# Kernel tuning notes

Measured on AMD Instinct MI355X. Metric: run time of the kernel, lower is better.

## Reference

```python
import jax, jax.numpy as jnp
import numpy as np

EMBED_DIM = 1152
NUM_HEADS = 16
HEAD_DIM = EMBED_DIM // NUM_HEADS
SCALE = HEAD_DIM ** -0.5


def setup_inputs() -> dict:
    key = jax.random.key(0)
    ks = jax.random.split(key, 9)
    B, N, D = 8, 1024, EMBED_DIM
    s = (2.0 / D) ** 0.5
    return {
        "hidden_states": jax.random.normal(ks[0], (B, N, D), dtype=jnp.float32),
        "q_w": jax.random.normal(ks[1], (D, D), dtype=jnp.float32) * s,
        "q_b": jnp.zeros((D,), dtype=jnp.float32),
        "k_w": jax.random.normal(ks[2], (D, D), dtype=jnp.float32) * s,
        "k_b": jnp.zeros((D,), dtype=jnp.float32),
        "v_w": jax.random.normal(ks[3], (D, D), dtype=jnp.float32) * s,
        "v_b": jnp.zeros((D,), dtype=jnp.float32),
        "o_w": jax.random.normal(ks[4], (D, D), dtype=jnp.float32) * s,
        "o_b": jnp.zeros((D,), dtype=jnp.float32),
    }


def reference(hidden_states, q_w, q_b, k_w, k_b, v_w, v_b, o_w, o_b):
    B, N, D = hidden_states.shape
    H, Hd = NUM_HEADS, HEAD_DIM
    # Linear layers: torch nn.Linear stores weight [out, in]; y = x @ W^T + b
    q = hidden_states @ q_w.T + q_b
    k = hidden_states @ k_w.T + k_b
    v = hidden_states @ v_w.T + v_b
    # [B, N, H, Hd] -> [B, H, N, Hd]
    q = q.reshape(B, N, H, Hd).transpose(0, 2, 1, 3)
    k = k.reshape(B, N, H, Hd).transpose(0, 2, 1, 3)
    v = v.reshape(B, N, H, Hd).transpose(0, 2, 1, 3)
    scores = jnp.einsum("bhqd,bhkd->bhqk", q, k) * SCALE
    attn_probs = jax.nn.softmax(scores, axis=-1)
    # dropout p=0.0 (eval) -> identity
    out = jnp.einsum("bhqk,bhkd->bhqd", attn_probs, v)
    out = out.transpose(0, 2, 1, 3).reshape(B, N, D)
    out = out @ o_w.T + o_b
    return (out, attn_probs)
```

## Files before the change

### kernel.cpp

```cpp
#include <hip/hip_runtime.h>

typedef _Float16 half_t;
typedef __attribute__((ext_vector_type(8))) _Float16 half8;
typedef __attribute__((ext_vector_type(4))) _Float16 half4;
typedef __attribute__((ext_vector_type(4))) float f32x4;

#define MFMA16(a, b, c) __builtin_amdgcn_mfma_f32_16x16x32_f16((a), (b), (c), 0, 0, 0)

__global__ void cvt_f16(const float* __restrict__ src, half_t* __restrict__ dst) {
  int i = (blockIdx.x * 256 + threadIdx.x) * 4;
  float4 v = *(const float4*)(src + i);
  half4 o = { (half_t)v.x, (half_t)v.y, (half_t)v.z, (half_t)v.w };
  *(half4*)(dst + i) = o;
}

__global__ __launch_bounds__(256, 2) void gemm_qkv(
    const half_t* __restrict__ X,
    const half_t* __restrict__ Wq, const half_t* __restrict__ Wk, const half_t* __restrict__ Wv,
    const float* __restrict__ bq, const float* __restrict__ bk, const float* __restrict__ bv,
    half_t* __restrict__ qo, half_t* __restrict__ ko, half_t* __restrict__ vo)
{
  __shared__ half_t As[128 * 40];
  __shared__ half_t Bs[128 * 40];
  const int t = threadIdx.x;
  const int w = t >> 6, L = t & 63, quad = L >> 4, c16 = L & 15;
  const int m0 = blockIdx.x * 128;
  const int by = blockIdx.y;
  const int mat = by / 9;
  const int f0 = (by - mat * 9) * 128;
  const half_t* W = (mat == 0) ? Wq : (mat == 1) ? Wk : Wv;
  const int mB = (w & 1) * 64, nB = (w >> 1) * 64;
  f32x4 acc[4][4] = {};
  for (int k0 = 0; k0 < 1152; k0 += 32) {
    __syncthreads();
    #pragma unroll
    for (int i = 0; i < 2; ++i) {
      int c = t + i * 256;
      int row = c >> 2, cc = (c & 3) * 8;
      *(half8*)&As[row * 40 + cc] = *(const half8*)&X[(m0 + row) * 1152 + k0 + cc];
      *(half8*)&Bs[row * 40 + cc] = *(const half8*)&W[(f0 + row) * 1152 + k0 + cc];
    }
    __syncthreads();
    half8 a[4], b[4];
    #pragma unroll
    for (int i = 0; i < 4; ++i) {
      a[i] = *(const half8*)&As[(mB + i * 16 + c16) * 40 + quad * 8];
      b[i] = *(const half8*)&Bs[(nB + i * 16 + c16) * 40 + quad * 8];
    }
    #pragma unroll
    for (int mt = 0; mt < 4; ++mt)
      #pragma unroll
      for (int nt = 0; nt < 4; ++nt)
        acc[mt][nt] = MFMA16(a[mt], b[nt], acc[mt][nt]);
  }
  const float* bias = (mat == 0) ? bq : (mat == 1) ? bk : bv;
  half_t* dst = (mat == 0) ? qo : (mat == 1) ? ko : vo;
  const float scl = (mat == 0) ? 0.11785113f : 1.0f;
  #pragma unroll
  for (int mt = 0; mt < 4; ++mt)
    #pragma unroll
    for (int nt = 0; nt < 4; ++nt) {
      int col = nB + nt * 16 + c16;
      int f = f0 + col;
      int h = f / 72, d = f - h * 72;
      float bb = bias[f];
      #pragma unroll
      for (int r = 0; r < 4; ++r) {
        int tok = m0 + mB + mt * 16 + quad * 4 + r;
        int b_ = tok >> 10, n = tok & 1023;
        dst[(((b_ * 16 + h) * 1024 + n) * 96) + d] = (half_t)((acc[mt][nt][r] + bb) * scl);
      }
    }
}

__global__ void transpose_v(const half_t* __restrict__ v, half_t* __restrict__ vt) {
  __shared__ half_t tile[64][73];
  const int t = threadIdx.x;
  const int bh = blockIdx.y;
  const int n0 = blockIdx.x * 64;
  #pragma unroll
  for (int i = 0; i < 18; ++i) {
    int flat = i * 256 + t;
    int n = flat / 72, d = flat - n * 72;
    tile[n][d] = v[(bh * 1024 + n0 + n) * 96 + d];
  }
  __syncthreads();
  #pragma unroll
  for (int i = 0; i < 18; ++i) {
    int flat = i * 256 + t;
    int d = flat >> 6, n = flat & 63;
    vt[(bh * 80 + d) * 1024 + n0 + n] = tile[n][d];
  }
}

__global__ __launch_bounds__(256, 2) void attn(
    const half_t* __restrict__ q_ws,
    const half_t* __restrict__ k_ws,
    const half_t* __restrict__ vt_ws,
    float* __restrict__ probs,
    half_t* __restrict__ ctx)
{
  __shared__ half_t Ks[32 * 104];
  __shared__ half_t Vts[80 * 40];
  __shared__ half_t Ps[4][32 * 40];
  const int t = threadIdx.x;
  const int w = t >> 6, L = t & 63, quad = L >> 4, c16 = L & 15;
  const int bh = blockIdx.y;
  const int qb = blockIdx.x * 128 + w * 32;
  const half_t* qp = q_ws + (bh * 1024 + qb) * 96;
  const half_t* kbase = k_ws + bh * 1024 * 96;
  const half_t* vtb = vt_ws + bh * 80 * 1024;

  half8 qf[2][3];
  #pragma unroll
  for (int mt = 0; mt < 2; ++mt)
    #pragma unroll
    for (int ks = 0; ks < 3; ++ks)
      qf[mt][ks] = *(const half8*)&qp[(mt * 16 + c16) * 96 + ks * 32 + quad * 8];

  float rsum[2][4] = {};
  for (int kt = 0; kt < 32; ++kt) {
    __syncthreads();
    for (int c = t; c < 384; c += 256) {
      int row = c / 12, cc = (c - row * 12) * 8;
      *(half8*)&Ks[row * 104 + cc] = *(const half8*)&kbase[(kt * 32 + row) * 96 + cc];
    }
    __syncthreads();
    #pragma unroll
    for (int nt = 0; nt < 2; ++nt) {
      half8 bf[3];
      #pragma unroll
      for (int ks = 0; ks < 3; ++ks)
        bf[ks] = *(const half8*)&Ks[(nt * 16 + c16) * 104 + ks * 32 + quad * 8];
      #pragma unroll
      for (int mt = 0; mt < 2; ++mt) {
        f32x4 s = {};
        #pragma unroll
        for (int ks = 0; ks < 3; ++ks) s = MFMA16(qf[mt][ks], bf[ks], s);
        #pragma unroll
        for (int r = 0; r < 4; ++r) rsum[mt][r] += __expf(s[r]);
      }
    }
  }
  float inv[2][4];
  #pragma unroll
  for (int mt = 0; mt < 2; ++mt)
    #pragma unroll
    for (int r = 0; r < 4; ++r) {
      float s = rsum[mt][r];
      s += __shfl_xor(s, 1); s += __shfl_xor(s, 2);
      s += __shfl_xor(s, 4); s += __shfl_xor(s, 8);
      inv[mt][r] = 1.0f / s;
    }

  f32x4 oacc[2][5] = {};
  float* pb = probs + ((long)bh * 1024 + qb) * 1024;
  for (int kt = 0; kt < 32; ++kt) {
    __syncthreads();
    for (int c = t; c < 384; c += 256) {
      int row = c / 12, cc = (c - row * 12) * 8;
      *(half8*)&Ks[row * 104 + cc] = *(const half8*)&kbase[(kt * 32 + row) * 96 + cc];
    }
    for (int c = t; c < 320; c += 256) {
      int row = c >> 2, cc = (c & 3) * 8;
      *(half8*)&Vts[row * 40 + cc] = *(const half8*)&vtb[row * 1024 + kt * 32 + cc];
    }
    __syncthreads();
    #pragma unroll
    for (int nt = 0; nt < 2; ++nt) {
      half8 bf[3];
      #pragma unroll
      for (int ks = 0; ks < 3; ++ks)
        bf[ks] = *(const half8*)&Ks[(nt * 16 + c16) * 104 + ks * 32 + quad * 8];
      #pragma unroll
      for (int mt = 0; mt < 2; ++mt) {
        f32x4 s = {};
        #pragma unroll
        for (int ks = 0; ks < 3; ++ks) s = MFMA16(qf[mt][ks], bf[ks], s);
        #pragma unroll
        for (int r = 0; r < 4; ++r) {
          float p = __expf(s[r]) * inv[mt][r];
          pb[(mt * 16 + quad * 4 + r) * 1024 + kt * 32 + nt * 16 + c16] = p;
          Ps[w][(mt * 16 + quad * 4 + r) * 40 + nt * 16 + c16] = (half_t)p;
        }
      }
    }
    __asm__ volatile("s_waitcnt lgkmcnt(0)" ::: "memory");
    #pragma unroll
    for (int mt = 0; mt < 2; ++mt) {
      half8 af = *(const half8*)&Ps[w][(mt * 16 + c16) * 40 + quad * 8];
      #pragma unroll
      for (int dt = 0; dt < 5; ++dt) {
        half8 bv = *(const half8*)&Vts[(dt * 16 + c16) * 40 + quad * 8];
        oacc[mt][dt] = MFMA16(af, bv, oacc[mt][dt]);
      }
    }
  }
  const int b_ = bh >> 4, h = bh & 15;
  #pragma unroll
  for (int mt = 0; mt < 2; ++mt)
    #pragma unroll
    for (int dt = 0; dt < 5; ++dt) {
      int d = dt * 16 + c16;
      if (d < 72) {
        #pragma unroll
        for (int r = 0; r < 4; ++r) {
          int q = qb + mt * 16 + quad * 4 + r;
          ctx[((b_ * 1024 + q) * 1152) + h * 72 + d] = (half_t)(oacc[mt][dt][r]);
        }
      }
    }
}

__global__ __launch_bounds__(256, 2) void gemm_o(
    const half_t* __restrict__ A, const half_t* __restrict__ W,
    const float* __restrict__ bias, float* __restrict__ out)
{
  __shared__ half_t As[128 * 40];
  __shared__ half_t Bs[128 * 40];
  const int t = threadIdx.x;
  const int w = t >> 6, L = t & 63, quad = L >> 4, c16 = L & 15;
  const int m0 = blockIdx.x * 128;
  const int f0 = blockIdx.y * 128;
  const int mB = (w & 1) * 64, nB = (w >> 1) * 64;
  f32x4 acc[4][4] = {};
  for (int k0 = 0; k0 < 1152; k0 += 32) {
    __syncthreads();
    #pragma unroll
    for (int i = 0; i < 2; ++i) {
      int c = t + i * 256;
      int row = c >> 2, cc = (c & 3) * 8;
      *(half8*)&As[row * 40 + cc] = *(const half8*)&A[(m0 + row) * 1152 + k0 + cc];
      *(half8*)&Bs[row * 40 + cc] = *(const half8*)&W[(f0 + row) * 1152 + k0 + cc];
    }
    __syncthreads();
    half8 a[4], b[4];
    #pragma unroll
    for (int i = 0; i < 4; ++i) {
      a[i] = *(const half8*)&As[(mB + i * 16 + c16) * 40 + quad * 8];
      b[i] = *(const half8*)&Bs[(nB + i * 16 + c16) * 40 + quad * 8];
    }
    #pragma unroll
    for (int mt = 0; mt < 4; ++mt)
      #pragma unroll
      for (int nt = 0; nt < 4; ++nt)
        acc[mt][nt] = MFMA16(a[mt], b[nt], acc[mt][nt]);
  }
  #pragma unroll
  for (int mt = 0; mt < 4; ++mt)
    #pragma unroll
    for (int nt = 0; nt < 4; ++nt) {
      int col = f0 + nB + nt * 16 + c16;
      float bb = bias[col];
      #pragma unroll
      for (int r = 0; r < 4; ++r) {
        int tok = m0 + mB + mt * 16 + quad * 4 + r;
        out[tok * 1152 + col] = acc[mt][nt][r] + bb;
      }
    }
}

extern "C" void kernel_launch(void* const* d_in, const int* in_sizes, int n_in,
                              void* d_out, int out_size, void* d_ws, size_t ws_size,
                              hipStream_t stream) {
  (void)in_sizes; (void)n_in; (void)out_size; (void)ws_size;
  const float* hidden = (const float*)d_in[0];
  const float* qw = (const float*)d_in[1];
  const float* qb = (const float*)d_in[2];
  const float* kw = (const float*)d_in[3];
  const float* kb = (const float*)d_in[4];
  const float* vw = (const float*)d_in[5];
  const float* vb = (const float*)d_in[6];
  const float* ow = (const float*)d_in[7];
  const float* ob = (const float*)d_in[8];
  float* out = (float*)d_out;
  float* probs = out + 9437184;

  half_t* ws  = (half_t*)d_ws;
  half_t* Xh  = ws;
  half_t* Wqh = Xh  + 9437184;
  half_t* Wkh = Wqh + 1327104;
  half_t* Wvh = Wkh + 1327104;
  half_t* Woh = Wvh + 1327104;
  half_t* Qw  = Woh + 1327104;
  half_t* Kw  = Qw  + 12582912;
  half_t* Vw  = Kw  + 12582912;
  half_t* Vt  = Vw  + 12582912;
  half_t* Ctx = Vt  + 10485760;

  hipMemsetAsync(Qw, 0, (size_t)12582912 * 2, stream);
  hipMemsetAsync(Kw, 0, (size_t)12582912 * 2, stream);
  hipMemsetAsync(Vt, 0, (size_t)10485760 * 2, stream);

  cvt_f16<<<9216, 256, 0, stream>>>(hidden, Xh);
  cvt_f16<<<1296, 256, 0, stream>>>(qw, Wqh);
  cvt_f16<<<1296, 256, 0, stream>>>(kw, Wkh);
  cvt_f16<<<1296, 256, 0, stream>>>(vw, Wvh);
  cvt_f16<<<1296, 256, 0, stream>>>(ow, Woh);

  gemm_qkv<<<dim3(64, 27), 256, 0, stream>>>(Xh, Wqh, Wkh, Wvh, qb, kb, vb, Qw, Kw, Vw);
  transpose_v<<<dim3(16, 128), 256, 0, stream>>>(Vw, Vt);
  attn<<<dim3(8, 128), 256, 0, stream>>>(Qw, Kw, Vt, probs, Ctx);
  gemm_o<<<dim3(64, 9), 256, 0, stream>>>(Ctx, Woh, ob, out);
}
```

Before: 1.017 ms.

## Use direct global-to-LDS loads in GEMMs, enlarge attention query tile, use exp2

```diff
diff --git a/kernel.cpp b/kernel.cpp
--- a/kernel.cpp
+++ b/kernel.cpp
@@ -6,6 +6,11 @@
 typedef __attribute__((ext_vector_type(4))) float f32x4;
 
 #define MFMA16(a, b, c) __builtin_amdgcn_mfma_f32_16x16x32_f16((a), (b), (c), 0, 0, 0)
+
+__device__ __forceinline__ void gld_lds16(const void* g, void* l) {
+  __builtin_amdgcn_global_load_lds((const __attribute__((address_space(1))) void*)g,
+                                   (__attribute__((address_space(3))) void*)l, 16, 0, 0);
+}
 
 __global__ void cvt_f16(const float* __restrict__ src, half_t* __restrict__ dst) {
   int i = (blockIdx.x * 256 + threadIdx.x) * 4;
@@ -20,8 +25,8 @@
     const float* __restrict__ bq, const float* __restrict__ bk, const float* __restrict__ bv,
     half_t* __restrict__ qo, half_t* __restrict__ ko, half_t* __restrict__ vo)
 {
-  __shared__ half_t As[128 * 40];
-  __shared__ half_t Bs[128 * 40];
+  __shared__ __align__(16) half_t As[128 * 32];
+  __shared__ __align__(16) half_t Bs[128 * 32];
   const int t = threadIdx.x;
   const int w = t >> 6, L = t & 63, quad = L >> 4, c16 = L & 15;
   const int m0 = blockIdx.x * 128;
@@ -35,17 +40,19 @@
     __syncthreads();
     #pragma unroll
     for (int i = 0; i < 2; ++i) {
-      int c = t + i * 256;
-      int row = c >> 2, cc = (c & 3) * 8;
-      *(half8*)&As[row * 40 + cc] = *(const half8*)&X[(m0 + row) * 1152 + k0 + cc];
-      *(half8*)&Bs[row * 40 + cc] = *(const half8*)&W[(f0 + row) * 1152 + k0 + cc];
+      int f = w * 2048 + i * 1024 + L * 16;
+      int row = f >> 6, colb = f & 63;
+      gld_lds16((const char*)&X[(m0 + row) * 1152 + k0] + colb,
+                (char*)As + w * 2048 + i * 1024);
+      gld_lds16((const char*)&W[(f0 + row) * 1152 + k0] + colb,
+                (char*)Bs + w * 2048 + i * 1024);
     }
     __syncthreads();
     half8 a[4], b[4];
     #pragma unroll
     for (int i = 0; i < 4; ++i) {
-      a[i] = *(const half8*)&As[(mB + i * 16 + c16) * 40 + quad * 8];
-      b[i] = *(const half8*)&Bs[(nB + i * 16 + c16) * 40 + quad * 8];
+      a[i] = *(const half8*)&As[(mB + i * 16 + c16) * 32 + quad * 8];
+      b[i] = *(const half8*)&Bs[(nB + i * 16 + c16) * 32 + quad * 8];
     }
     #pragma unroll
     for (int mt = 0; mt < 4; ++mt)
@@ -55,7 +62,7 @@
   }
   const float* bias = (mat == 0) ? bq : (mat == 1) ? bk : bv;
   half_t* dst = (mat == 0) ? qo : (mat == 1) ? ko : vo;
-  const float scl = (mat == 0) ? 0.11785113f : 1.0f;
+  const float scl = (mat == 0) ? 0.17002322f : 1.0f;
   #pragma unroll
   for (int mt = 0; mt < 4; ++mt)
     #pragma unroll
@@ -102,23 +109,23 @@
 {
   __shared__ half_t Ks[32 * 104];
   __shared__ half_t Vts[80 * 40];
-  __shared__ half_t Ps[4][32 * 40];
+  __shared__ half_t Ps[4][64 * 40];
   const int t = threadIdx.x;
   const int w = t >> 6, L = t & 63, quad = L >> 4, c16 = L & 15;
   const int bh = blockIdx.y;
-  const int qb = blockIdx.x * 128 + w * 32;
+  const int qb = blockIdx.x * 256 + w * 64;
   const half_t* qp = q_ws + (bh * 1024 + qb) * 96;
   const half_t* kbase = k_ws + bh * 1024 * 96;
   const half_t* vtb = vt_ws + bh * 80 * 1024;
 
-  half8 qf[2][3];
-  #pragma unroll
-  for (int mt = 0; mt < 2; ++mt)
+  half8 qf[4][3];
+  #pragma unroll
+  for (int mt = 0; mt < 4; ++mt)
     #pragma unroll
     for (int ks = 0; ks < 3; ++ks)
       qf[mt][ks] = *(const half8*)&qp[(mt * 16 + c16) * 96 + ks * 32 + quad * 8];
 
-  float rsum[2][4] = {};
+  float rsum[4][4] = {};
   for (int kt = 0; kt < 32; ++kt) {
     __syncthreads();
     for (int c = t; c < 384; c += 256) {
@@ -133,18 +140,18 @@
       for (int ks = 0; ks < 3; ++ks)
         bf[ks] = *(const half8*)&Ks[(nt * 16 + c16) * 104 + ks * 32 + quad * 8];
       #pragma unroll
-      for (int mt = 0; mt < 2; ++mt) {
+      for (int mt = 0; mt < 4; ++mt) {
         f32x4 s = {};
         #pragma unroll
         for (int ks = 0; ks < 3; ++ks) s = MFMA16(qf[mt][ks], bf[ks], s);
         #pragma unroll
-        for (int r = 0; r < 4; ++r) rsum[mt][r] += __expf(s[r]);
-      }
-    }
-  }
-  float inv[2][4];
-  #pragma unroll
-  for (int mt = 0; mt < 2; ++mt)
+        for (int r = 0; r < 4; ++r) rsum[mt][r] += __builtin_amdgcn_exp2f(s[r]);
+      }
+    }
+  }
+  float inv[4][4];
+  #pragma unroll
+  for (int mt = 0; mt < 4; ++mt)
     #pragma unroll
     for (int r = 0; r < 4; ++r) {
       float s = rsum[mt][r];
@@ -153,7 +160,7 @@
       inv[mt][r] = 1.0f / s;
     }
 
-  f32x4 oacc[2][5] = {};
+  f32x4 oacc[4][5] = {};
   float* pb = probs + ((long)bh * 1024 + qb) * 1024;
   for (int kt = 0; kt < 32; ++kt) {
     __syncthreads();
@@ -173,32 +180,34 @@
       for (int ks = 0; ks < 3; ++ks)
         bf[ks] = *(const half8*)&Ks[(nt * 16 + c16) * 104 + ks * 32 + quad * 8];
       #pragma unroll
-      for (int mt = 0; mt < 2; ++mt) {
+      for (int mt = 0; mt < 4; ++mt) {
         f32x4 s = {};
         #pragma unroll
         for (int ks = 0; ks < 3; ++ks) s = MFMA16(qf[mt][ks], bf[ks], s);
         #pragma unroll
         for (int r = 0; r < 4; ++r) {
-          float p = __expf(s[r]) * inv[mt][r];
+          float p = __builtin_amdgcn_exp2f(s[r]) * inv[mt][r];
           pb[(mt * 16 + quad * 4 + r) * 1024 + kt * 32 + nt * 16 + c16] = p;
           Ps[w][(mt * 16 + quad * 4 + r) * 40 + nt * 16 + c16] = (half_t)p;
         }
       }
     }
     __asm__ volatile("s_waitcnt lgkmcnt(0)" ::: "memory");
-    #pragma unroll
-    for (int mt = 0; mt < 2; ++mt) {
+    half8 bv[5];
+    #pragma unroll
+    for (int dt = 0; dt < 5; ++dt)
+      bv[dt] = *(const half8*)&Vts[(dt * 16 + c16) * 40 + quad * 8];
+    #pragma unroll
+    for (int mt = 0; mt < 4; ++mt) {
       half8 af = *(const half8*)&Ps[w][(mt * 16 + c16) * 40 + quad * 8];
       #pragma unroll
-      for (int dt = 0; dt < 5; ++dt) {
-        half8 bv = *(const half8*)&Vts[(dt * 16 + c16) * 40 + quad * 8];
-        oacc[mt][dt] = MFMA16(af, bv, oacc[mt][dt]);
-      }
+      for (int dt = 0; dt < 5; ++dt)
+        oacc[mt][dt] = MFMA16(af, bv[dt], oacc[mt][dt]);
     }
   }
   const int b_ = bh >> 4, h = bh & 15;
   #pragma unroll
-  for (int mt = 0; mt < 2; ++mt)
+  for (int mt = 0; mt < 4; ++mt)
     #pragma unroll
     for (int dt = 0; dt < 5; ++dt) {
       int d = dt * 16 + c16;
@@ -216,8 +225,8 @@
     const half_t* __restrict__ A, const half_t* __restrict__ W,
     const float* __restrict__ bias, float* __restrict__ out)
 {
-  __shared__ half_t As[128 * 40];
-  __shared__ half_t Bs[128 * 40];
+  __shared__ __align__(16) half_t As[128 * 32];
+  __shared__ __align__(16) half_t Bs[128 * 32];
   const int t = threadIdx.x;
   const int w = t >> 6, L = t & 63, quad = L >> 4, c16 = L & 15;
   const int m0 = blockIdx.x * 128;
@@ -228,17 +237,19 @@
     __syncthreads();
     #pragma unroll
     for (int i = 0; i < 2; ++i) {
-      int c = t + i * 256;
-      int row = c >> 2, cc = (c & 3) * 8;
-      *(half8*)&As[row * 40 + cc] = *(const half8*)&A[(m0 + row) * 1152 + k0 + cc];
-      *(half8*)&Bs[row * 40 + cc] = *(const half8*)&W[(f0 + row) * 1152 + k0 + cc];
+      int f = w * 2048 + i * 1024 + L * 16;
+      int row = f >> 6, colb = f & 63;
+      gld_lds16((const char*)&A[(m0 + row) * 1152 + k0] + colb,
+                (char*)As + w * 2048 + i * 1024);
+      gld_lds16((const char*)&W[(f0 + row) * 1152 + k0] + colb,
+                (char*)Bs + w * 2048 + i * 1024);
     }
     __syncthreads();
     half8 a[4], b[4];
     #pragma unroll
     for (int i = 0; i < 4; ++i) {
-      a[i] = *(const half8*)&As[(mB + i * 16 + c16) * 40 + quad * 8];
-      b[i] = *(const half8*)&Bs[(nB + i * 16 + c16) * 40 + quad * 8];
+      a[i] = *(const half8*)&As[(mB + i * 16 + c16) * 32 + quad * 8];
+      b[i] = *(const half8*)&Bs[(nB + i * 16 + c16) * 32 + quad * 8];
     }
     #pragma unroll
     for (int mt = 0; mt < 4; ++mt)
@@ -300,6 +311,6 @@
 
   gemm_qkv<<<dim3(64, 27), 256, 0, stream>>>(Xh, Wqh, Wkh, Wvh, qb, kb, vb, Qw, Kw, Vw);
   transpose_v<<<dim3(16, 128), 256, 0, stream>>>(Vw, Vt);
-  attn<<<dim3(8, 128), 256, 0, stream>>>(Qw, Kw, Vt, probs, Ctx);
+  attn<<<dim3(4, 128), 256, 0, stream>>>(Qw, Kw, Vt, probs, Ctx);
   gemm_o<<<dim3(64, 9), 256, 0, stream>>>(Ctx, Woh, ob, out);
 }
```

New measurement: 970.3 us. 1.05x faster.
